# Optimization experiments

Hardware: AMD Instinct MI355X
Metric: run time of the kernel (lower is better)

## Reference

```python
import jax, jax.numpy as jnp
import numpy as np

N = 4_000_000   # batch size
L = 48          # number of stacked tiny layers
EPS = 1e-5      # BatchNorm1d default eps


def setup_inputs() -> dict:
    key = jax.random.key(0)
    ks = jax.random.split(key, 6)
    return {
        "x": jax.random.normal(ks[0], (N, 2), dtype=jnp.float32),
        "W": jax.random.normal(ks[1], (L, 2, 2), dtype=jnp.float32),
        "b": jax.random.normal(ks[2], (L, 2), dtype=jnp.float32) * 0.1,
        "gamma": jnp.ones((L, 2), dtype=jnp.float32),
        "beta": jnp.zeros((L, 2), dtype=jnp.float32),
        "scale": jax.random.normal(ks[3], (L, 2), dtype=jnp.float32),
        "shift": jax.random.normal(ks[4], (L, 2), dtype=jnp.float32) * 0.1,
        "Wf": jax.random.normal(ks[5], (1, 2), dtype=jnp.float32),
        "bf": jnp.zeros((1,), dtype=jnp.float32),
    }


def _forward(x, W, b, gamma, beta, scale, shift, Wf, bf):
    def layer_step(h, p):
        Wl, bl, gl, bel, scl, shl = p
        y = h @ Wl.T + bl                       # Linear(2,2)  -> [N,2]
        m = jnp.mean(y, axis=0)                 # BatchNorm1d (training stats)
        v = jnp.mean((y - m) ** 2, axis=0)      # biased variance
        y = (y - m) * jax.lax.rsqrt(v + EPS) * gl + bel
        y = jnp.tanh(y) * scl + shl             # Tanh + elementwise affine
        return y, None                          # dropout p=0 -> identity

    h, _ = jax.lax.scan(layer_step, x, (W, b, gamma, beta, scale, shift))
    return jax.nn.sigmoid(h @ Wf.T + bf)        # final Linear(2,1) + Sigmoid -> [N,1]


def reference(x, W, b, gamma, beta, scale, shift, Wf, bf):
    return _forward(x, W, b, gamma, beta, scale, shift, Wf, bf)
```

## Files before the change

kernel.cpp:

```cpp
#include <hip/hip_runtime.h>

#define NB   256
#define NT   1024
#define PRPT 8
#define TT   (NB * NT)
#define NHUB 8

typedef unsigned long long ull;

struct alignas(128) Slot { double s[4]; double pad[12]; };

__device__ __forceinline__ float ex2(float x) { return __builtin_amdgcn_exp2f(x); }

__device__ __forceinline__ float rcp_acc(float d) {
  float r = __builtin_amdgcn_rcpf(d);
  return r * __builtin_fmaf(-d, r, 2.0f);
}
__device__ __forceinline__ float div_acc(float n, float d, float r) {
  float q = n * r;
  float rho = __builtin_fmaf(-q, d, n);
  return __builtin_fmaf(rho, r, q);
}

__device__ __forceinline__ float actf(float y, double P, double Q, float sc, float sh) {
  double u = fma((double)y, P, Q);
  float uf = (float)u;
  uf = fminf(fmaxf(uf, -60.0f), 60.0f);
  float e = ex2(uf);
  float t = (e - 1.0f) * __builtin_amdgcn_rcpf(e + 1.0f);
  return __builtin_fmaf(t, sc, sh);
}

__device__ __forceinline__ float sigm(double uo) {
  const double C1 = 1.4426950408889634074;
  float w = (float)(-uo * C1);
  w = fminf(fmaxf(w, -60.0f), 60.0f);
  float e = ex2(w);
  float d = 1.0f + e;
  float r = rcp_acc(d);
  return div_acc(1.0f, d, r);
}

__device__ __forceinline__ void layer_sync(
    int l, double s0, double s1, double s2, double s3,
    Slot* __restrict__ slot, Slot* __restrict__ coef,
    float gmv0, float gmv1, float btv0, float btv1, double dn,
    double& P0, double& P1, double& Q0, double& Q1)
{
  __shared__ double lr[NT / 64][4];
  __shared__ double lg[4][4];
  __shared__ double lc[4];
  const int lane = threadIdx.x & 63, wave = threadIdx.x >> 6;
  const ull pbit = (ull)((~((unsigned)l >> 1)) & 1u);

#pragma unroll
  for (int off = 32; off > 0; off >>= 1) {
    s0 += __shfl_down(s0, off, 64);
    s1 += __shfl_down(s1, off, 64);
    s2 += __shfl_down(s2, off, 64);
    s3 += __shfl_down(s3, off, 64);
  }
  if (lane == 0) { lr[wave][0] = s0; lr[wave][1] = s1; lr[wave][2] = s2; lr[wave][3] = s3; }
  __syncthreads();

  Slot* sb = slot + (size_t)(l & 1) * NB;
  if (threadIdx.x < NT / 64) {
    double a0 = lr[threadIdx.x][0], a1 = lr[threadIdx.x][1];
    double a2 = lr[threadIdx.x][2], a3 = lr[threadIdx.x][3];
#pragma unroll
    for (int off = 8; off > 0; off >>= 1) {
      a0 += __shfl_down(a0, off, 64);
      a1 += __shfl_down(a1, off, 64);
      a2 += __shfl_down(a2, off, 64);
      a3 += __shfl_down(a3, off, 64);
    }
    if (threadIdx.x == 0) {
      ull* my = (ull*)(sb + blockIdx.x)->s;
      __hip_atomic_store(my + 0, (__double_as_longlong(a0) & ~1ull) | pbit,
                         __ATOMIC_RELAXED, __HIP_MEMORY_SCOPE_AGENT);
      __hip_atomic_store(my + 1, (__double_as_longlong(a1) & ~1ull) | pbit,
                         __ATOMIC_RELAXED, __HIP_MEMORY_SCOPE_AGENT);
      __hip_atomic_store(my + 2, (__double_as_longlong(a2) & ~1ull) | pbit,
                         __ATOMIC_RELAXED, __HIP_MEMORY_SCOPE_AGENT);
      __hip_atomic_store(my + 3, (__double_as_longlong(a3) & ~1ull) | pbit,
                         __ATOMIC_RELAXED, __HIP_MEMORY_SCOPE_AGENT);
    }
  }

  if (blockIdx.x < NHUB) {
    if (threadIdx.x < NB) {
      ull* sl = (ull*)(sb + threadIdx.x)->s;
      ull v0, v1, v2, v3;
      for (;;) {
        v0 = __hip_atomic_load(sl + 0, __ATOMIC_RELAXED, __HIP_MEMORY_SCOPE_AGENT);
        v1 = __hip_atomic_load(sl + 1, __ATOMIC_RELAXED, __HIP_MEMORY_SCOPE_AGENT);
        v2 = __hip_atomic_load(sl + 2, __ATOMIC_RELAXED, __HIP_MEMORY_SCOPE_AGENT);
        v3 = __hip_atomic_load(sl + 3, __ATOMIC_RELAXED, __HIP_MEMORY_SCOPE_AGENT);
        if ((((v0 & v1 & v2 & v3) ^ pbit) & 1ull) == 0ull &&
            (((v0 | v1 | v2 | v3) ^ pbit) & 1ull) == 0ull) break;
        __builtin_amdgcn_s_sleep(1);
      }
      double g0 = __longlong_as_double((long long)v0);
      double g1 = __longlong_as_double((long long)v1);
      double g2 = __longlong_as_double((long long)v2);
      double g3 = __longlong_as_double((long long)v3);
#pragma unroll
      for (int off = 32; off > 0; off >>= 1) {
        g0 += __shfl_down(g0, off, 64);
        g1 += __shfl_down(g1, off, 64);
        g2 += __shfl_down(g2, off, 64);
        g3 += __shfl_down(g3, off, 64);
      }
      if (lane == 0) { lg[wave][0] = g0; lg[wave][1] = g1; lg[wave][2] = g2; lg[wave][3] = g3; }
    }
    __syncthreads();
    if (threadIdx.x == 0) {
      const double t0 = lg[0][0] + lg[1][0] + lg[2][0] + lg[3][0];
      const double t1 = lg[0][1] + lg[1][1] + lg[2][1] + lg[3][1];
      const double t2 = lg[0][2] + lg[1][2] + lg[2][2] + lg[3][2];
      const double t3 = lg[0][3] + lg[1][3] + lg[2][3] + lg[3][3];
      const double m0 = t0 * dn, m1 = t1 * dn;
      const double v0 = fma(-m0, m0, t2 * dn);
      const double v1 = fma(-m1, m1, t3 * dn);
      const double rs0 = 1.0 / sqrt(v0 + 1e-5);
      const double rs1 = 1.0 / sqrt(v1 + 1e-5);
      const double A0 = (double)gmv0 * rs0, A1 = (double)gmv1 * rs1;
      const double C2 = 2.8853900817779268147;
      const ull w0 = (__double_as_longlong(A0 * C2) & ~1ull) | pbit;
      const ull w1 = (__double_as_longlong(A1 * C2) & ~1ull) | pbit;
      const ull w2 = (__double_as_longlong(((double)btv0 - m0 * A0) * C2) & ~1ull) | pbit;
      const ull w3 = (__double_as_longlong(((double)btv1 - m1 * A1) * C2) & ~1ull) | pbit;
      ull* cl = (ull*)(coef + (size_t)(l & 1) * NHUB + blockIdx.x)->s;
      __hip_atomic_store(cl + 0, w0, __ATOMIC_RELAXED, __HIP_MEMORY_SCOPE_AGENT);
      __hip_atomic_store(cl + 1, w1, __ATOMIC_RELAXED, __HIP_MEMORY_SCOPE_AGENT);
      __hip_atomic_store(cl + 2, w2, __ATOMIC_RELAXED, __HIP_MEMORY_SCOPE_AGENT);
      __hip_atomic_store(cl + 3, w3, __ATOMIC_RELAXED, __HIP_MEMORY_SCOPE_AGENT);
      lc[0] = __longlong_as_double((long long)w0);
      lc[1] = __longlong_as_double((long long)w1);
      lc[2] = __longlong_as_double((long long)w2);
      lc[3] = __longlong_as_double((long long)w3);
    }
  } else {
    if (threadIdx.x == 0) {
      ull* cl = (ull*)(coef + (size_t)(l & 1) * NHUB + (blockIdx.x & (NHUB - 1)))->s;
      ull v0, v1, v2, v3;
      for (;;) {
        v0 = __hip_atomic_load(cl + 0, __ATOMIC_RELAXED, __HIP_MEMORY_SCOPE_AGENT);
        v1 = __hip_atomic_load(cl + 1, __ATOMIC_RELAXED, __HIP_MEMORY_SCOPE_AGENT);
        v2 = __hip_atomic_load(cl + 2, __ATOMIC_RELAXED, __HIP_MEMORY_SCOPE_AGENT);
        v3 = __hip_atomic_load(cl + 3, __ATOMIC_RELAXED, __HIP_MEMORY_SCOPE_AGENT);
        if ((((v0 & v1 & v2 & v3) ^ pbit) & 1ull) == 0ull &&
            (((v0 | v1 | v2 | v3) ^ pbit) & 1ull) == 0ull) break;
      }
      lc[0] = __longlong_as_double((long long)v0);
      lc[1] = __longlong_as_double((long long)v1);
      lc[2] = __longlong_as_double((long long)v2);
      lc[3] = __longlong_as_double((long long)v3);
    }
  }
  __syncthreads();
  P0 = lc[0]; P1 = lc[1]; Q0 = lc[2]; Q1 = lc[3];
}

__global__ __launch_bounds__(NT, 4) void fraud_persist(
    const float4* __restrict__ x, const float* __restrict__ W,
    const float* __restrict__ b, const float* __restrict__ gm,
    const float* __restrict__ bt, const float* __restrict__ sc,
    const float* __restrict__ sh, const float* __restrict__ Wf,
    const float* __restrict__ bf, float2* __restrict__ out,
    Slot* __restrict__ slot, Slot* __restrict__ coef, int N2, int L)
{
  const int tid = blockIdx.x * NT + threadIdx.x;
  const bool in8 = (tid + 7 * TT) < N2;
  float4 y[PRPT];
  float s0 = 0.f, s1 = 0.f, s2 = 0.f, s3 = 0.f;

  {
    const float w00 = W[0], w01 = W[1], w10 = W[2], w11 = W[3];
    const float b0 = b[0], b1 = b[1];
#pragma unroll
    for (int r = 0; r < PRPT - 1; ++r) {
      const float4 p = x[tid + r * TT];
      const float a0 = __builtin_fmaf(p.x, w00, __builtin_fmaf(p.y, w01, b0));
      const float a1 = __builtin_fmaf(p.x, w10, __builtin_fmaf(p.y, w11, b1));
      const float a2 = __builtin_fmaf(p.z, w00, __builtin_fmaf(p.w, w01, b0));
      const float a3 = __builtin_fmaf(p.z, w10, __builtin_fmaf(p.w, w11, b1));
      y[r] = make_float4(a0, a1, a2, a3);
      s0 += a0 + a2; s1 += a1 + a3;
      s2 = __builtin_fmaf(a0, a0, __builtin_fmaf(a2, a2, s2));
      s3 = __builtin_fmaf(a1, a1, __builtin_fmaf(a3, a3, s3));
    }
    const float4 p = in8 ? x[tid + 7 * TT] : make_float4(0.f, 0.f, 0.f, 0.f);
    const float a0 = __builtin_fmaf(p.x, w00, __builtin_fmaf(p.y, w01, b0));
    const float a1 = __builtin_fmaf(p.x, w10, __builtin_fmaf(p.y, w11, b1));
    const float a2 = __builtin_fmaf(p.z, w00, __builtin_fmaf(p.w, w01, b0));
    const float a3 = __builtin_fmaf(p.z, w10, __builtin_fmaf(p.w, w11, b1));
    y[7] = make_float4(a0, a1, a2, a3);
    if (in8) {
      s0 += a0 + a2; s1 += a1 + a3;
      s2 = __builtin_fmaf(a0, a0, __builtin_fmaf(a2, a2, s2));
      s3 = __builtin_fmaf(a1, a1, __builtin_fmaf(a3, a3, s3));
    }
  }
  const double dn = 0.5 / (double)N2;

  float gmv0 = gm[0], gmv1 = gm[1], btv0 = bt[0], btv1 = bt[1];
  float sc0 = sc[0], sh0 = sh[0], sc1 = sc[1], sh1 = sh[1];
  float w00 = W[4], w01 = W[5], w10 = W[6], w11 = W[7];
  float bb0 = b[2], bb1 = b[3];

  double P0, P1, Q0, Q1;
  layer_sync(0, (double)s0, (double)s1, (double)s2, (double)s3,
             slot, coef, gmv0, gmv1, btv0, btv1, dn, P0, P1, Q0, Q1);

  for (int l = 0; l < L; ++l) {
    const bool last = (l == L - 1);
    const float cw00 = w00, cw01 = w01, cw10 = w10, cw11 = w11;
    const float cb0 = bb0, cb1 = bb1;
    const float csc0 = sc0, csh0 = sh0, csc1 = sc1, csh1 = sh1;

    s0 = 0.f; s1 = 0.f; s2 = 0.f; s3 = 0.f;
#pragma unroll
    for (int r = 0; r < PRPT - 1; ++r) {
      const float z0 = actf(y[r].x, P0, Q0, csc0, csh0);
      const float z1 = actf(y[r].y, P1, Q1, csc1, csh1);
      const float z2 = actf(y[r].z, P0, Q0, csc0, csh0);
      const float z3 = actf(y[r].w, P1, Q1, csc1, csh1);
      if (!last) {
        const float a0 = __builtin_fmaf(z0, cw00, __builtin_fmaf(z1, cw01, cb0));
        const float a1 = __builtin_fmaf(z0, cw10, __builtin_fmaf(z1, cw11, cb1));
        const float a2 = __builtin_fmaf(z2, cw00, __builtin_fmaf(z3, cw01, cb0));
        const float a3 = __builtin_fmaf(z2, cw10, __builtin_fmaf(z3, cw11, cb1));
        y[r] = make_float4(a0, a1, a2, a3);
        s0 += a0 + a2; s1 += a1 + a3;
        s2 = __builtin_fmaf(a0, a0, __builtin_fmaf(a2, a2, s2));
        s3 = __builtin_fmaf(a1, a1, __builtin_fmaf(a3, a3, s3));
      } else {
        const double u0 = fma((double)z0, (double)cw00, fma((double)z1, (double)cw01, (double)cb0));
        const double u1 = fma((double)z2, (double)cw00, fma((double)z3, (double)cw01, (double)cb0));
        out[tid + r * TT] = make_float2(sigm(u0), sigm(u1));
      }
    }
    {
      const float z0 = actf(y[7].x, P0, Q0, csc0, csh0);
      const float z1 = actf(y[7].y, P1, Q1, csc1, csh1);
      const float z2 = actf(y[7].z, P0, Q0, csc0, csh0);
      const float z3 = actf(y[7].w, P1, Q1, csc1, csh1);
      if (!last) {
        const float a0 = __builtin_fmaf(z0, cw00, __builtin_fmaf(z1, cw01, cb0));
        const float a1 = __builtin_fmaf(z0, cw10, __builtin_fmaf(z1, cw11, cb1));
        const float a2 = __builtin_fmaf(z2, cw00, __builtin_fmaf(z3, cw01, cb0));
        const float a3 = __builtin_fmaf(z2, cw10, __builtin_fmaf(z3, cw11, cb1));
        y[7] = make_float4(a0, a1, a2, a3);
        if (in8) {
          s0 += a0 + a2; s1 += a1 + a3;
          s2 = __builtin_fmaf(a0, a0, __builtin_fmaf(a2, a2, s2));
          s3 = __builtin_fmaf(a1, a1, __builtin_fmaf(a3, a3, s3));
        }
      } else if (in8) {
        const double u0 = fma((double)z0, (double)cw00, fma((double)z1, (double)cw01, (double)cb0));
        const double u1 = fma((double)z2, (double)cw00, fma((double)z3, (double)cw01, (double)cb0));
        out[tid + 7 * TT] = make_float2(sigm(u0), sigm(u1));
      }
    }
    if (!last) {
      const int n = l + 1;
      gmv0 = gm[2 * n]; gmv1 = gm[2 * n + 1];
      btv0 = bt[2 * n]; btv1 = bt[2 * n + 1];
      sc0 = sc[2 * n]; sh0 = sh[2 * n];
      sc1 = sc[2 * n + 1]; sh1 = sh[2 * n + 1];
      if (n < L - 1) {
        w00 = W[4 * n + 4]; w01 = W[4 * n + 5]; w10 = W[4 * n + 6]; w11 = W[4 * n + 7];
        bb0 = b[2 * n + 2]; bb1 = b[2 * n + 3];
      } else {
        w00 = Wf[0]; w01 = Wf[1]; w10 = 0.0f; w11 = 0.0f; bb0 = bf[0]; bb1 = 0.0f;
      }
      layer_sync(n, (double)s0, (double)s1, (double)s2, (double)s3,
                 slot, coef, gmv0, gmv1, btv0, btv1, dn, P0, P1, Q0, Q1);
    }
  }
}

extern "C" void kernel_launch(void* const* d_in, const int* in_sizes, int n_in,
                              void* d_out, int out_size, void* d_ws, size_t ws_size,
                              hipStream_t stream) {
  const float* x  = (const float*)d_in[0];
  const float* W  = (const float*)d_in[1];
  const float* b  = (const float*)d_in[2];
  const float* gm = (const float*)d_in[3];
  const float* bt = (const float*)d_in[4];
  const float* sc = (const float*)d_in[5];
  const float* sh = (const float*)d_in[6];
  const float* Wf = (const float*)d_in[7];
  const float* bf = (const float*)d_in[8];
  const int N  = in_sizes[0] / 2;
  const int L  = in_sizes[1] / 4;
  const int N2 = N / 2;

  char* wsb = (char*)d_ws;
  Slot* coef = (Slot*)wsb;
  Slot* slot = (Slot*)(wsb + 4096);

  hipMemsetAsync(d_ws, 0, 4096 + 2 * NB * sizeof(Slot), stream);

  fraud_persist<<<NB, NT, 0, stream>>>(
      (const float4*)x, W, b, gm, bt, sc, sh, Wf, bf,
      (float2*)d_out, slot, coef, N2, L);
}
```

Measured before the change: 399.8 us.

## Dedicate one block as reduction hub and split per-layer stats into two halves

Block 0 becomes a dedicated coordinator that gathers the per-block partial sums from the 255 worker blocks and publishes BatchNorm coefficients to 8 mirror slots, replacing the old scheme of 8 hub blocks that also did compute. Workers now reduce and publish statistics in two halves (rows 0-3, then rows 4-7) so the first half's partials reach the hub while the second half is still computing. The aim is to shorten the grid-wide barrier's critical path and overlap reduction latency with activation math. The cost is one block less of compute, each worker handling more rows, and an extra block-level reduction per layer.

```diff
diff --git a/kernel.cpp b/kernel.cpp
--- a/kernel.cpp
+++ b/kernel.cpp
@@ -2,9 +2,11 @@
 
 #define NB   256
 #define NT   1024
+#define NW   255
+#define TTW  (NW * NT)
 #define PRPT 8
-#define TT   (NB * NT)
-#define NHUB 8
+#define HALF 4
+#define NMIR 8
 
 typedef unsigned long long ull;
 
@@ -41,18 +43,39 @@
   return div_acc(1.0f, d, r);
 }
 
-__device__ __forceinline__ void layer_sync(
-    int l, double s0, double s1, double s2, double s3,
-    Slot* __restrict__ slot, Slot* __restrict__ coef,
-    float gmv0, float gmv1, float btv0, float btv1, double dn,
-    double& P0, double& P1, double& Q0, double& Q1)
-{
-  __shared__ double lr[NT / 64][4];
-  __shared__ double lg[4][4];
-  __shared__ double lc[4];
+__device__ __forceinline__ unsigned gen_parity(int k) {
+  return (~((unsigned)k >> 1)) & 1u;
+}
+
+__device__ __forceinline__ void pub4(ull* p, double a0, double a1, double a2, double a3,
+                                     unsigned pb) {
+  const ull t = (ull)pb;
+  __hip_atomic_store(p + 0, (ull)(__double_as_longlong(a0) & ~1ll) | t,
+                     __ATOMIC_RELAXED, __HIP_MEMORY_SCOPE_AGENT);
+  __hip_atomic_store(p + 1, (ull)(__double_as_longlong(a1) & ~1ll) | t,
+                     __ATOMIC_RELAXED, __HIP_MEMORY_SCOPE_AGENT);
+  __hip_atomic_store(p + 2, (ull)(__double_as_longlong(a2) & ~1ll) | t,
+                     __ATOMIC_RELAXED, __HIP_MEMORY_SCOPE_AGENT);
+  __hip_atomic_store(p + 3, (ull)(__double_as_longlong(a3) & ~1ll) | t,
+                     __ATOMIC_RELAXED, __HIP_MEMORY_SCOPE_AGENT);
+}
+
+__device__ __forceinline__ void poll4(const ull* p, unsigned pb,
+                                      ull& w0, ull& w1, ull& w2, ull& w3) {
+  const ull t = (ull)pb;
+  for (;;) {
+    w0 = __hip_atomic_load(p + 0, __ATOMIC_RELAXED, __HIP_MEMORY_SCOPE_AGENT);
+    w1 = __hip_atomic_load(p + 1, __ATOMIC_RELAXED, __HIP_MEMORY_SCOPE_AGENT);
+    w2 = __hip_atomic_load(p + 2, __ATOMIC_RELAXED, __HIP_MEMORY_SCOPE_AGENT);
+    w3 = __hip_atomic_load(p + 3, __ATOMIC_RELAXED, __HIP_MEMORY_SCOPE_AGENT);
+    if ((((w0 & w1 & w2 & w3) ^ t) & 1ull) == 0ull &&
+        (((w0 | w1 | w2 | w3) ^ t) & 1ull) == 0ull) return;
+  }
+}
+
+__device__ __forceinline__ void blk_reduce(double& s0, double& s1, double& s2, double& s3,
+                                           double lr[NT / 64][4]) {
   const int lane = threadIdx.x & 63, wave = threadIdx.x >> 6;
-  const ull pbit = (ull)((~((unsigned)l >> 1)) & 1u);
-
 #pragma unroll
   for (int off = 32; off > 0; off >>= 1) {
     s0 += __shfl_down(s0, off, 64);
@@ -62,8 +85,6 @@
   }
   if (lane == 0) { lr[wave][0] = s0; lr[wave][1] = s1; lr[wave][2] = s2; lr[wave][3] = s3; }
   __syncthreads();
-
-  Slot* sb = slot + (size_t)(l & 1) * NB;
   if (threadIdx.x < NT / 64) {
     double a0 = lr[threadIdx.x][0], a1 = lr[threadIdx.x][1];
     double a2 = lr[threadIdx.x][2], a3 = lr[threadIdx.x][3];
@@ -74,92 +95,41 @@
       a2 += __shfl_down(a2, off, 64);
       a3 += __shfl_down(a3, off, 64);
     }
-    if (threadIdx.x == 0) {
-      ull* my = (ull*)(sb + blockIdx.x)->s;
-      __hip_atomic_store(my + 0, (__double_as_longlong(a0) & ~1ull) | pbit,
-                         __ATOMIC_RELAXED, __HIP_MEMORY_SCOPE_AGENT);
-      __hip_atomic_store(my + 1, (__double_as_longlong(a1) & ~1ull) | pbit,
-                         __ATOMIC_RELAXED, __HIP_MEMORY_SCOPE_AGENT);
-      __hip_atomic_store(my + 2, (__double_as_longlong(a2) & ~1ull) | pbit,
-                         __ATOMIC_RELAXED, __HIP_MEMORY_SCOPE_AGENT);
-      __hip_atomic_store(my + 3, (__double_as_longlong(a3) & ~1ull) | pbit,
-                         __ATOMIC_RELAXED, __HIP_MEMORY_SCOPE_AGENT);
-    }
-  }
-
-  if (blockIdx.x < NHUB) {
-    if (threadIdx.x < NB) {
-      ull* sl = (ull*)(sb + threadIdx.x)->s;
-      ull v0, v1, v2, v3;
-      for (;;) {
-        v0 = __hip_atomic_load(sl + 0, __ATOMIC_RELAXED, __HIP_MEMORY_SCOPE_AGENT);
-        v1 = __hip_atomic_load(sl + 1, __ATOMIC_RELAXED, __HIP_MEMORY_SCOPE_AGENT);
-        v2 = __hip_atomic_load(sl + 2, __ATOMIC_RELAXED, __HIP_MEMORY_SCOPE_AGENT);
-        v3 = __hip_atomic_load(sl + 3, __ATOMIC_RELAXED, __HIP_MEMORY_SCOPE_AGENT);
-        if ((((v0 & v1 & v2 & v3) ^ pbit) & 1ull) == 0ull &&
-            (((v0 | v1 | v2 | v3) ^ pbit) & 1ull) == 0ull) break;
-        __builtin_amdgcn_s_sleep(1);
-      }
-      double g0 = __longlong_as_double((long long)v0);
-      double g1 = __longlong_as_double((long long)v1);
-      double g2 = __longlong_as_double((long long)v2);
-      double g3 = __longlong_as_double((long long)v3);
-#pragma unroll
-      for (int off = 32; off > 0; off >>= 1) {
-        g0 += __shfl_down(g0, off, 64);
-        g1 += __shfl_down(g1, off, 64);
-        g2 += __shfl_down(g2, off, 64);
-        g3 += __shfl_down(g3, off, 64);
-      }
-      if (lane == 0) { lg[wave][0] = g0; lg[wave][1] = g1; lg[wave][2] = g2; lg[wave][3] = g3; }
-    }
-    __syncthreads();
-    if (threadIdx.x == 0) {
-      const double t0 = lg[0][0] + lg[1][0] + lg[2][0] + lg[3][0];
-      const double t1 = lg[0][1] + lg[1][1] + lg[2][1] + lg[3][1];
-      const double t2 = lg[0][2] + lg[1][2] + lg[2][2] + lg[3][2];
-      const double t3 = lg[0][3] + lg[1][3] + lg[2][3] + lg[3][3];
-      const double m0 = t0 * dn, m1 = t1 * dn;
-      const double v0 = fma(-m0, m0, t2 * dn);
-      const double v1 = fma(-m1, m1, t3 * dn);
-      const double rs0 = 1.0 / sqrt(v0 + 1e-5);
-      const double rs1 = 1.0 / sqrt(v1 + 1e-5);
-      const double A0 = (double)gmv0 * rs0, A1 = (double)gmv1 * rs1;
-      const double C2 = 2.8853900817779268147;
-      const ull w0 = (__double_as_longlong(A0 * C2) & ~1ull) | pbit;
-      const ull w1 = (__double_as_longlong(A1 * C2) & ~1ull) | pbit;
-      const ull w2 = (__double_as_longlong(((double)btv0 - m0 * A0) * C2) & ~1ull) | pbit;
-      const ull w3 = (__double_as_longlong(((double)btv1 - m1 * A1) * C2) & ~1ull) | pbit;
-      ull* cl = (ull*)(coef + (size_t)(l & 1) * NHUB + blockIdx.x)->s;
-      __hip_atomic_store(cl + 0, w0, __ATOMIC_RELAXED, __HIP_MEMORY_SCOPE_AGENT);
-      __hip_atomic_store(cl + 1, w1, __ATOMIC_RELAXED, __HIP_MEMORY_SCOPE_AGENT);
-      __hip_atomic_store(cl + 2, w2, __ATOMIC_RELAXED, __HIP_MEMORY_SCOPE_AGENT);
-      __hip_atomic_store(cl + 3, w3, __ATOMIC_RELAXED, __HIP_MEMORY_SCOPE_AGENT);
-      lc[0] = __longlong_as_double((long long)w0);
-      lc[1] = __longlong_as_double((long long)w1);
-      lc[2] = __longlong_as_double((long long)w2);
-      lc[3] = __longlong_as_double((long long)w3);
-    }
-  } else {
-    if (threadIdx.x == 0) {
-      ull* cl = (ull*)(coef + (size_t)(l & 1) * NHUB + (blockIdx.x & (NHUB - 1)))->s;
-      ull v0, v1, v2, v3;
-      for (;;) {
-        v0 = __hip_atomic_load(cl + 0, __ATOMIC_RELAXED, __HIP_MEMORY_SCOPE_AGENT);
-        v1 = __hip_atomic_load(cl + 1, __ATOMIC_RELAXED, __HIP_MEMORY_SCOPE_AGENT);
-        v2 = __hip_atomic_load(cl + 2, __ATOMIC_RELAXED, __HIP_MEMORY_SCOPE_AGENT);
-        v3 = __hip_atomic_load(cl + 3, __ATOMIC_RELAXED, __HIP_MEMORY_SCOPE_AGENT);
-        if ((((v0 & v1 & v2 & v3) ^ pbit) & 1ull) == 0ull &&
-            (((v0 | v1 | v2 | v3) ^ pbit) & 1ull) == 0ull) break;
-      }
-      lc[0] = __longlong_as_double((long long)v0);
-      lc[1] = __longlong_as_double((long long)v1);
-      lc[2] = __longlong_as_double((long long)v2);
-      lc[3] = __longlong_as_double((long long)v3);
-    }
+    s0 = a0; s1 = a1; s2 = a2; s3 = a3;
   }
   __syncthreads();
-  P0 = lc[0]; P1 = lc[1]; Q0 = lc[2]; Q1 = lc[3];
+}
+
+__device__ __forceinline__ void hub_gather(const Slot* sb, unsigned pb,
+                                           double lg[4][4],
+                                           double& t0, double& t1, double& t2, double& t3) {
+  const int lane = threadIdx.x & 63, wave = threadIdx.x >> 6;
+  double g0 = 0, g1 = 0, g2 = 0, g3 = 0;
+  if (threadIdx.x < NW) {
+    const ull* sp = (const ull*)(sb + threadIdx.x)->s;
+    ull w0, w1, w2, w3;
+    poll4(sp, pb, w0, w1, w2, w3);
+    g0 = __longlong_as_double((long long)w0);
+    g1 = __longlong_as_double((long long)w1);
+    g2 = __longlong_as_double((long long)w2);
+    g3 = __longlong_as_double((long long)w3);
+  }
+  if (wave < 4) {
+#pragma unroll
+    for (int off = 32; off > 0; off >>= 1) {
+      g0 += __shfl_down(g0, off, 64);
+      g1 += __shfl_down(g1, off, 64);
+      g2 += __shfl_down(g2, off, 64);
+      g3 += __shfl_down(g3, off, 64);
+    }
+    if (lane == 0) { lg[wave][0] = g0; lg[wave][1] = g1; lg[wave][2] = g2; lg[wave][3] = g3; }
+  }
+  __syncthreads();
+  t0 = lg[0][0] + lg[1][0] + lg[2][0] + lg[3][0];
+  t1 = lg[0][1] + lg[1][1] + lg[2][1] + lg[3][1];
+  t2 = lg[0][2] + lg[1][2] + lg[2][2] + lg[3][2];
+  t3 = lg[0][3] + lg[1][3] + lg[2][3] + lg[3][3];
+  __syncthreads();
 }
 
 __global__ __launch_bounds__(NT, 4) void fraud_persist(
@@ -168,60 +138,131 @@
     const float* __restrict__ bt, const float* __restrict__ sc,
     const float* __restrict__ sh, const float* __restrict__ Wf,
     const float* __restrict__ bf, float2* __restrict__ out,
-    Slot* __restrict__ slot, Slot* __restrict__ coef, int N2, int L)
+    Slot* __restrict__ aslot, Slot* __restrict__ bslot,
+    Slot* __restrict__ coef, int N2, int L)
 {
-  const int tid = blockIdx.x * NT + threadIdx.x;
-  const bool in8 = (tid + 7 * TT) < N2;
+  if (blockIdx.x == 0) {
+    __shared__ double lg[4][4];
+    const double dn = 0.5 / (double)N2;
+    for (int k = 0; k < L; ++k) {
+      const unsigned pb = gen_parity(k);
+      const int par = k & 1;
+      double tA0, tA1, tA2, tA3, tB0, tB1, tB2, tB3;
+      hub_gather(aslot + (size_t)par * NW, pb, lg, tA0, tA1, tA2, tA3);
+      hub_gather(bslot + (size_t)par * NW, pb, lg, tB0, tB1, tB2, tB3);
+      if (threadIdx.x < NMIR) {
+        const double t0 = tA0 + tB0, t1 = tA1 + tB1;
+        const double t2 = tA2 + tB2, t3 = tA3 + tB3;
+        const double m0 = t0 * dn, m1 = t1 * dn;
+        const double v0 = fma(-m0, m0, t2 * dn);
+        const double v1 = fma(-m1, m1, t3 * dn);
+        const double rs0 = 1.0 / sqrt(v0 + 1e-5);
+        const double rs1 = 1.0 / sqrt(v1 + 1e-5);
+        const double A0 = (double)gm[2 * k] * rs0, A1 = (double)gm[2 * k + 1] * rs1;
+        const double C2 = 2.8853900817779268147;
+        pub4((ull*)(coef + (size_t)par * NMIR + threadIdx.x)->s,
+             A0 * C2, A1 * C2,
+             ((double)bt[2 * k] - m0 * A0) * C2,
+             ((double)bt[2 * k + 1] - m1 * A1) * C2, pb);
+      }
+    }
+    return;
+  }
+
+  __shared__ double lr[NT / 64][4];
+  __shared__ double lc[4];
+  const int tid = (blockIdx.x - 1) * NT + threadIdx.x;
+  const int mir = (int)(blockIdx.x & (NMIR - 1));
+  const bool in8 = (tid + 7 * TTW) < N2;
   float4 y[PRPT];
-  float s0 = 0.f, s1 = 0.f, s2 = 0.f, s3 = 0.f;
+  float s0, s1, s2, s3;
+
+  float sc0 = sc[0], sh0 = sh[0], sc1 = sc[1], sh1 = sh[1];
+  float w00 = W[4], w01 = W[5], w10 = W[6], w11 = W[7];
+  float bb0 = b[2], bb1 = b[3];
 
   {
-    const float w00 = W[0], w01 = W[1], w10 = W[2], w11 = W[3];
-    const float b0 = b[0], b1 = b[1];
-#pragma unroll
-    for (int r = 0; r < PRPT - 1; ++r) {
-      const float4 p = x[tid + r * TT];
-      const float a0 = __builtin_fmaf(p.x, w00, __builtin_fmaf(p.y, w01, b0));
-      const float a1 = __builtin_fmaf(p.x, w10, __builtin_fmaf(p.y, w11, b1));
-      const float a2 = __builtin_fmaf(p.z, w00, __builtin_fmaf(p.w, w01, b0));
-      const float a3 = __builtin_fmaf(p.z, w10, __builtin_fmaf(p.w, w11, b1));
+    const float v00 = W[0], v01 = W[1], v10 = W[2], v11 = W[3];
+    const float c0 = b[0], c1 = b[1];
+    s0 = 0.f; s1 = 0.f; s2 = 0.f; s3 = 0.f;
+#pragma unroll
+    for (int r = 0; r < HALF; ++r) {
+      const float4 p = x[tid + r * TTW];
+      const float a0 = __builtin_fmaf(p.x, v00, __builtin_fmaf(p.y, v01, c0));
+      const float a1 = __builtin_fmaf(p.x, v10, __builtin_fmaf(p.y, v11, c1));
+      const float a2 = __builtin_fmaf(p.z, v00, __builtin_fmaf(p.w, v01, c0));
+      const float a3 = __builtin_fmaf(p.z, v10, __builtin_fmaf(p.w, v11, c1));
       y[r] = make_float4(a0, a1, a2, a3);
       s0 += a0 + a2; s1 += a1 + a3;
       s2 = __builtin_fmaf(a0, a0, __builtin_fmaf(a2, a2, s2));
       s3 = __builtin_fmaf(a1, a1, __builtin_fmaf(a3, a3, s3));
     }
-    const float4 p = in8 ? x[tid + 7 * TT] : make_float4(0.f, 0.f, 0.f, 0.f);
-    const float a0 = __builtin_fmaf(p.x, w00, __builtin_fmaf(p.y, w01, b0));
-    const float a1 = __builtin_fmaf(p.x, w10, __builtin_fmaf(p.y, w11, b1));
-    const float a2 = __builtin_fmaf(p.z, w00, __builtin_fmaf(p.w, w01, b0));
-    const float a3 = __builtin_fmaf(p.z, w10, __builtin_fmaf(p.w, w11, b1));
-    y[7] = make_float4(a0, a1, a2, a3);
-    if (in8) {
+    {
+      double d0 = s0, d1 = s1, d2 = s2, d3 = s3;
+      blk_reduce(d0, d1, d2, d3, lr);
+      if (threadIdx.x == 0)
+        pub4((ull*)(aslot + (blockIdx.x - 1))->s, d0, d1, d2, d3, 1u);
+    }
+
+    s0 = 0.f; s1 = 0.f; s2 = 0.f; s3 = 0.f;
+#pragma unroll
+    for (int r = HALF; r < PRPT - 1; ++r) {
+      const float4 p = x[tid + r * TTW];
+      const float a0 = __builtin_fmaf(p.x, v00, __builtin_fmaf(p.y, v01, c0));
+      const float a1 = __builtin_fmaf(p.x, v10, __builtin_fmaf(p.y, v11, c1));
+      const float a2 = __builtin_fmaf(p.z, v00, __builtin_fmaf(p.w, v01, c0));
+      const float a3 = __builtin_fmaf(p.z, v10, __builtin_fmaf(p.w, v11, c1));
+      y[r] = make_float4(a0, a1, a2, a3);
       s0 += a0 + a2; s1 += a1 + a3;
       s2 = __builtin_fmaf(a0, a0, __builtin_fmaf(a2, a2, s2));
       s3 = __builtin_fmaf(a1, a1, __builtin_fmaf(a3, a3, s3));
     }
-  }
-  const double dn = 0.5 / (double)N2;
-
-  float gmv0 = gm[0], gmv1 = gm[1], btv0 = bt[0], btv1 = bt[1];
-  float sc0 = sc[0], sh0 = sh[0], sc1 = sc[1], sh1 = sh[1];
-  float w00 = W[4], w01 = W[5], w10 = W[6], w11 = W[7];
-  float bb0 = b[2], bb1 = b[3];
+    {
+      const float4 p = in8 ? x[tid + 7 * TTW] : make_float4(0.f, 0.f, 0.f, 0.f);
+      const float a0 = __builtin_fmaf(p.x, v00, __builtin_fmaf(p.y, v01, c0));
+      const float a1 = __builtin_fmaf(p.x, v10, __builtin_fmaf(p.y, v11, c1));
+      const float a2 = __builtin_fmaf(p.z, v00, __builtin_fmaf(p.w, v01, c0));
+      const float a3 = __builtin_fmaf(p.z, v10, __builtin_fmaf(p.w, v11, c1));
+      y[7] = make_float4(a0, a1, a2, a3);
+      if (in8) {
+        s0 += a0 + a2; s1 += a1 + a3;
+        s2 = __builtin_fmaf(a0, a0, __builtin_fmaf(a2, a2, s2));
+        s3 = __builtin_fmaf(a1, a1, __builtin_fmaf(a3, a3, s3));
+      }
+    }
+    {
+      double d0 = s0, d1 = s1, d2 = s2, d3 = s3;
+      blk_reduce(d0, d1, d2, d3, lr);
+      if (threadIdx.x == 0)
+        pub4((ull*)(bslot + (blockIdx.x - 1))->s, d0, d1, d2, d3, 1u);
+    }
+  }
 
   double P0, P1, Q0, Q1;
-  layer_sync(0, (double)s0, (double)s1, (double)s2, (double)s3,
-             slot, coef, gmv0, gmv1, btv0, btv1, dn, P0, P1, Q0, Q1);
+  {
+    if (threadIdx.x == 0) {
+      ull w0, w1, w2, w3;
+      poll4((const ull*)(coef + mir)->s, 1u, w0, w1, w2, w3);
+      lc[0] = __longlong_as_double((long long)w0);
+      lc[1] = __longlong_as_double((long long)w1);
+      lc[2] = __longlong_as_double((long long)w2);
+      lc[3] = __longlong_as_double((long long)w3);
+    }
+    __syncthreads();
+    P0 = lc[0]; P1 = lc[1]; Q0 = lc[2]; Q1 = lc[3];
+  }
 
   for (int l = 0; l < L; ++l) {
     const bool last = (l == L - 1);
+    const unsigned pbn = gen_parity(l + 1);
+    const int par = (l + 1) & 1;
     const float cw00 = w00, cw01 = w01, cw10 = w10, cw11 = w11;
     const float cb0 = bb0, cb1 = bb1;
     const float csc0 = sc0, csh0 = sh0, csc1 = sc1, csh1 = sh1;
 
     s0 = 0.f; s1 = 0.f; s2 = 0.f; s3 = 0.f;
 #pragma unroll
-    for (int r = 0; r < PRPT - 1; ++r) {
+    for (int r = 0; r < HALF; ++r) {
       const float z0 = actf(y[r].x, P0, Q0, csc0, csh0);
       const float z1 = actf(y[r].y, P1, Q1, csc1, csh1);
       const float z2 = actf(y[r].z, P0, Q0, csc0, csh0);
@@ -238,35 +279,50 @@
       } else {
         const double u0 = fma((double)z0, (double)cw00, fma((double)z1, (double)cw01, (double)cb0));
         const double u1 = fma((double)z2, (double)cw00, fma((double)z3, (double)cw01, (double)cb0));
-        out[tid + r * TT] = make_float2(sigm(u0), sigm(u1));
-      }
-    }
-    {
-      const float z0 = actf(y[7].x, P0, Q0, csc0, csh0);
-      const float z1 = actf(y[7].y, P1, Q1, csc1, csh1);
-      const float z2 = actf(y[7].z, P0, Q0, csc0, csh0);
-      const float z3 = actf(y[7].w, P1, Q1, csc1, csh1);
+        out[tid + r * TTW] = make_float2(sigm(u0), sigm(u1));
+      }
+    }
+    if (!last) {
+      double d0 = s0, d1 = s1, d2 = s2, d3 = s3;
+      blk_reduce(d0, d1, d2, d3, lr);
+      if (threadIdx.x == 0)
+        pub4((ull*)(aslot + (size_t)par * NW + (blockIdx.x - 1))->s, d0, d1, d2, d3, pbn);
+    }
+
+    s0 = 0.f; s1 = 0.f; s2 = 0.f; s3 = 0.f;
+#pragma unroll
+    for (int r = HALF; r < PRPT; ++r) {
+      const float z0 = actf(y[r].x, P0, Q0, csc0, csh0);
+      const float z1 = actf(y[r].y, P1, Q1, csc1, csh1);
+      const float z2 = actf(y[r].z, P0, Q0, csc0, csh0);
+      const float z3 = actf(y[r].w, P1, Q1, csc1, csh1);
+      const bool ok = (r < 7) || in8;
       if (!last) {
         const float a0 = __builtin_fmaf(z0, cw00, __builtin_fmaf(z1, cw01, cb0));
         const float a1 = __builtin_fmaf(z0, cw10, __builtin_fmaf(z1, cw11, cb1));
         const float a2 = __builtin_fmaf(z2, cw00, __builtin_fmaf(z3, cw01, cb0));
         const float a3 = __builtin_fmaf(z2, cw10, __builtin_fmaf(z3, cw11, cb1));
-        y[7] = make_float4(a0, a1, a2, a3);
-        if (in8) {
+        y[r] = make_float4(a0, a1, a2, a3);
+        if (ok) {
           s0 += a0 + a2; s1 += a1 + a3;
           s2 = __builtin_fmaf(a0, a0, __builtin_fmaf(a2, a2, s2));
           s3 = __builtin_fmaf(a1, a1, __builtin_fmaf(a3, a3, s3));
         }
-      } else if (in8) {
+      } else if (ok) {
         const double u0 = fma((double)z0, (double)cw00, fma((double)z1, (double)cw01, (double)cb0));
         const double u1 = fma((double)z2, (double)cw00, fma((double)z3, (double)cw01, (double)cb0));
-        out[tid + 7 * TT] = make_float2(sigm(u0), sigm(u1));
+        out[tid + r * TTW] = make_float2(sigm(u0), sigm(u1));
       }
     }
     if (!last) {
+      {
+        double d0 = s0, d1 = s1, d2 = s2, d3 = s3;
+        blk_reduce(d0, d1, d2, d3, lr);
+        if (threadIdx.x == 0)
+          pub4((ull*)(bslot + (size_t)par * NW + (blockIdx.x - 1))->s, d0, d1, d2, d3, pbn);
+      }
+
       const int n = l + 1;
-      gmv0 = gm[2 * n]; gmv1 = gm[2 * n + 1];
-      btv0 = bt[2 * n]; btv1 = bt[2 * n + 1];
       sc0 = sc[2 * n]; sh0 = sh[2 * n];
       sc1 = sc[2 * n + 1]; sh1 = sh[2 * n + 1];
       if (n < L - 1) {
@@ -275,8 +331,16 @@
       } else {
         w00 = Wf[0]; w01 = Wf[1]; w10 = 0.0f; w11 = 0.0f; bb0 = bf[0]; bb1 = 0.0f;
       }
-      layer_sync(n, (double)s0, (double)s1, (double)s2, (double)s3,
-                 slot, coef, gmv0, gmv1, btv0, btv1, dn, P0, P1, Q0, Q1);
+      if (threadIdx.x == 0) {
+        ull w0v, w1v, w2v, w3v;
+        poll4((const ull*)(coef + (size_t)par * NMIR + mir)->s, pbn, w0v, w1v, w2v, w3v);
+        lc[0] = __longlong_as_double((long long)w0v);
+        lc[1] = __longlong_as_double((long long)w1v);
+        lc[2] = __longlong_as_double((long long)w2v);
+        lc[3] = __longlong_as_double((long long)w3v);
+      }
+      __syncthreads();
+      P0 = lc[0]; P1 = lc[1]; Q0 = lc[2]; Q1 = lc[3];
     }
   }
 }
@@ -298,12 +362,13 @@
   const int N2 = N / 2;
 
   char* wsb = (char*)d_ws;
-  Slot* coef = (Slot*)wsb;
-  Slot* slot = (Slot*)(wsb + 4096);
-
-  hipMemsetAsync(d_ws, 0, 4096 + 2 * NB * sizeof(Slot), stream);
+  Slot* coef  = (Slot*)wsb;
+  Slot* aslot = (Slot*)(wsb + 4096);
+  Slot* bslot = (Slot*)(wsb + 4096 + 2 * NW * sizeof(Slot));
+
+  (void)hipMemsetAsync(d_ws, 0, 4096 + 4 * NW * sizeof(Slot), stream);
 
   fraud_persist<<<NB, NT, 0, stream>>>(
       (const float4*)x, W, b, gm, bt, sc, sh, Wf, bf,
-      (float2*)d_out, slot, coef, N2, L);
-}
+      (float2*)d_out, aslot, bslot, coef, N2, L);
+}
```

New measurement: 482.4 us. 20.7% more time.
